# Kernel optimization log

Hardware: AMD Instinct MI355X
Metric: run time of the kernel (lower is better)

The kernel has to match this reference:

```python
import jax, jax.numpy as jnp
import numpy as np

LATENT = 128
K = 1024          # num_embeddings
LENGTH = 128
HID = 200         # LSTM hidden
IN = 768
COND = 1536


def setup_inputs() -> dict:
    key = jax.random.key(0)
    ks = jax.random.split(key, 16)
    B = 256
    x = jax.random.normal(ks[0], (B, 1, LENGTH, IN), dtype=jnp.float32)
    condition = jax.random.normal(ks[1], (B, 1, LENGTH, COND), dtype=jnp.float32)
    noise = jax.random.normal(ks[2], (B, IN), dtype=jnp.float32)
    s = 0.05
    # LSTM params (PyTorch gate order: i, f, g, o)
    W_ih = jax.random.normal(ks[3], (4 * HID, IN), dtype=jnp.float32) * s
    W_hh = jax.random.normal(ks[4], (4 * HID, HID), dtype=jnp.float32) * s
    b_ih = jax.random.normal(ks[5], (4 * HID,), dtype=jnp.float32) * s
    b_hh = jax.random.normal(ks[6], (4 * HID,), dtype=jnp.float32) * s
    # encoder fc: HID -> LATENT
    W_enc = jax.random.normal(ks[7], (LATENT, HID), dtype=jnp.float32) * s
    b_enc = jnp.zeros((LATENT,), dtype=jnp.float32)
    # codebook, uniform(-1/K, 1/K) as in the module
    emb = jax.random.uniform(ks[8], (K, LATENT), minval=-1.0 / K, maxval=1.0 / K, dtype=jnp.float32)
    # decoder MLP
    D1_IN = LATENT + COND + IN  # 2432
    W1 = jax.random.normal(ks[9], (200, D1_IN), dtype=jnp.float32) * s
    b1 = jnp.zeros((200,), dtype=jnp.float32)
    W2 = jax.random.normal(ks[10], (400, 200), dtype=jnp.float32) * s
    b2 = jnp.zeros((400,), dtype=jnp.float32)
    W3 = jax.random.normal(ks[11], (IN, 400), dtype=jnp.float32) * s
    b3 = jnp.zeros((IN,), dtype=jnp.float32)
    return {"x": x, "condition": condition, "noise": noise,
            "W_ih": W_ih, "W_hh": W_hh, "b_ih": b_ih, "b_hh": b_hh,
            "W_enc": W_enc, "b_enc": b_enc, "emb": emb,
            "W1": W1, "b1": b1, "W2": W2, "b2": b2, "W3": W3, "b3": b3}


def _lstm_last_h(xs, W_ih, W_hh, b_ih, b_hh):
    # xs: [B, T, IN] -> final hidden state [B, HID]
    B = xs.shape[0]
    h0 = jnp.zeros((B, HID), dtype=xs.dtype)
    c0 = jnp.zeros((B, HID), dtype=xs.dtype)
    # precompute input projections for all timesteps: [T, B, 4H]
    gates_x = jnp.einsum('bti,gi->tbg', xs, W_ih) + b_ih + b_hh

    def step(carry, gx):
        h, c = carry
        g = gx + h @ W_hh.T  # [B, 4H]
        i, f, gg, o = jnp.split(g, 4, axis=-1)
        c = jax.nn.sigmoid(f) * c + jax.nn.sigmoid(i) * jnp.tanh(gg)
        h = jax.nn.sigmoid(o) * jnp.tanh(c)
        return (h, c), None

    (h, _), _ = jax.lax.scan(step, (h0, c0), gates_x)
    return h


def reference(x, condition, noise, W_ih, W_hh, b_ih, b_hh, W_enc, b_enc, emb,
              W1, b1, W2, b2, W3, b3):
    B = x.shape[0]
    # Encoder
    xs = x.reshape(B, -1, IN)                      # [B, T, 768]
    h = _lstm_last_h(xs, W_ih, W_hh, b_ih, b_hh)   # [B, 200]
    z_e = h @ W_enc.T + b_enc                      # [B, latent]
    # VectorQuantizer: squared-distance argmin + gather
    d = (jnp.sum(z_e * z_e, axis=-1, keepdims=True)
         + jnp.sum(emb * emb, axis=1)
         - 2.0 * z_e @ emb.T)                      # [B, K]
    indices = jnp.argmin(d, axis=-1)               # [B]
    z_q = emb[indices]                             # [B, latent]
    # Decoder (forward uses z_q directly)
    L = LENGTH
    z = jnp.broadcast_to(z_q[:, None, None, :], (B, 1, L, LATENT))
    n = jnp.broadcast_to(noise[:, None, None, :], (B, 1, L, IN))
    zc = jnp.concatenate([z, condition, n], axis=-1)  # [B,1,L,2432]
    h1 = jax.nn.relu(zc @ W1.T + b1)
    h2 = jax.nn.relu(h1 @ W2.T + b2)
    out = jax.nn.sigmoid(h2 @ W3.T + b3)
    return out.reshape(-1, 1, L, IN)
```

## Files before the change

### kernel.cpp

```cpp
#include <hip/hip_runtime.h>
#include <hip/hip_fp16.h>
#include <math.h>

typedef unsigned short u16;
typedef u16 u16x8 __attribute__((ext_vector_type(8)));
typedef __bf16 bf16x8 __attribute__((ext_vector_type(8)));
typedef float f32x4 __attribute__((ext_vector_type(4)));

#define HID 200
#define G4H 800
#define TLEN 128
#define LATENT 128
#define NCODES 1024
#define DIN 768
#define DCOND 1536
#define NB 256
#define MROWS (NB * TLEN)
#define LDG 896
#define LDH1 256
#define LDH2 512
#define NOUT 768

__device__ __forceinline__ u16 f2b(float f) {
  union { float f; unsigned u; } v; v.f = f;
  unsigned r = v.u + 0x7fffu + ((v.u >> 16) & 1u);
  return (u16)(r >> 16);
}
__device__ __forceinline__ float b2f(u16 h) {
  union { unsigned u; float f; } v; v.u = ((unsigned)h) << 16;
  return v.f;
}
__device__ __forceinline__ float sigf(float x) { return 1.f / (1.f + __expf(-x)); }
__device__ __forceinline__ float tanh_fast(float x) {
  return 1.f - 2.f / (__expf(2.f * x) + 1.f);
}

__device__ __forceinline__ void gl16(const void* g, void* l) {
  __builtin_amdgcn_global_load_lds(
      (const __attribute__((address_space(1))) void*)g,
      (__attribute__((address_space(3))) void*)l, 16, 0, 0);
}

__device__ __forceinline__ unsigned cvtpk(float a, float b) {
  unsigned r;
  asm("v_cvt_pk_bf16_f32 %0, %1, %2" : "=v"(r) : "v"(a), "v"(b));
  return r;
}

__global__ void cvt_pad(const float* __restrict__ src, u16* __restrict__ dst,
                        int nr, int nc, int lds, int col0, int NRp, int KP) {
  int i = blockIdx.x * blockDim.x + threadIdx.x;
  if (i >= NRp * KP) return;
  int r = i / KP, c = i - r * KP;
  float v = (r < nr && c < nc) ? src[(size_t)r * lds + col0 + c] : 0.f;
  dst[i] = f2b(v);
}

__global__ void pad_f32(const float* __restrict__ src, float* __restrict__ dst,
                        int n, int npad) {
  int i = blockIdx.x * blockDim.x + threadIdx.x;
  if (i < npad) dst[i] = (i < n) ? src[i] : 0.f;
}

__global__ void pack_whh(const float* __restrict__ Whh, __half2* __restrict__ Wt2,
                         const float* __restrict__ b_ih, const float* __restrict__ b_hh,
                         float* __restrict__ biasc) {
  int i = blockIdx.x * blockDim.x + threadIdx.x;
  if (i < 200 * 400) {
    int k = i / 400, r = i - k * 400;
    Wt2[i] = __floats2half2_rn(Whh[(size_t)r * HID + k], Whh[(size_t)(r + 400) * HID + k]);
  }
  if (i < G4H) biasc[i] = b_ih[i] + b_hh[i];
}

enum { EPI_GATES = 0, EPI_H1 = 1, EPI_H2 = 2, EPI_OUT = 3 };

__device__ __forceinline__ f32x4 mfma16(bf16x8 a, bf16x8 b, f32x4 c) {
  return __builtin_amdgcn_mfma_f32_16x16x32_bf16(a, b, c, 0, 0, 0);
}

template<bool AF32, int EPI>
__global__ __launch_bounds__(256) void gemm_bf16(
    const void* __restrict__ Ap, const u16* __restrict__ Bp,
    void* __restrict__ Cp, int K, int ldc, const float* __restrict__ bias) {
  __shared__ __attribute__((aligned(16))) char AsRaw[AF32 ? 128 * 32 * 4 : 128 * 32 * 2];
  __shared__ __attribute__((aligned(16))) u16 Bs[128 * 32];
  float* Asf = (float*)AsRaw;
  u16* As16 = (u16*)AsRaw;

  const int t = threadIdx.x;
  const int tileN = blockIdx.x * 128;
  const int tileM = blockIdx.y * 128;
  const int l = t & 63;
  const int w = t >> 6;
  const int wr = (w >> 1) * 64;
  const int wc = (w & 1) * 64;
  const int fr = l & 15;
  const int fg = l >> 4;

  const u16* bsrc[2];
  u16* bdst[2];
#pragma unroll
  for (int j = 0; j < 2; ++j) {
    int tb = w * 1024 + j * 4096 + (t & 63) * 16;
    int row = tb >> 6, gd = (tb >> 4) & 3;
    bsrc[j] = Bp + (size_t)(tileN + row) * K + ((gd ^ ((row >> 1) & 3)) << 3);
    bdst[j] = Bs + w * 512 + j * 2048;
  }
  const float* asrcF[4];
  float* adstF[4];
  const u16* asrcH[2];
  u16* adstH[2];
  if constexpr (AF32) {
#pragma unroll
    for (int j = 0; j < 4; ++j) {
      int tb = w * 1024 + j * 4096 + (t & 63) * 16;
      int row = tb >> 7, gd = (tb >> 4) & 7;
      asrcF[j] = (const float*)Ap + (size_t)(tileM + row) * K + ((gd ^ (row & 7)) << 2);
      adstF[j] = Asf + w * 256 + j * 1024;
    }
  } else {
#pragma unroll
    for (int j = 0; j < 2; ++j) {
      int tb = w * 1024 + j * 4096 + (t & 63) * 16;
      int row = tb >> 6, gd = (tb >> 4) & 3;
      asrcH[j] = (const u16*)Ap + (size_t)(tileM + row) * K + ((gd ^ ((row >> 1) & 3)) << 3);
      adstH[j] = As16 + w * 512 + j * 2048;
    }
  }

  f32x4 acc[4][4];
#pragma unroll
  for (int m = 0; m < 4; ++m)
#pragma unroll
    for (int n = 0; n < 4; ++n) {
      f32x4 z = {0.f, 0.f, 0.f, 0.f};
      acc[m][n] = z;
    }

  for (int k0 = 0; k0 < K; k0 += 32) {
#pragma unroll
    for (int j = 0; j < 2; ++j) { gl16(bsrc[j], bdst[j]); bsrc[j] += 32; }
    if constexpr (AF32) {
#pragma unroll
      for (int j = 0; j < 4; ++j) { gl16(asrcF[j], adstF[j]); asrcF[j] += 32; }
    } else {
#pragma unroll
      for (int j = 0; j < 2; ++j) { gl16(asrcH[j], adstH[j]); asrcH[j] += 32; }
    }
    __syncthreads();

    bf16x8 av[4], bv[4];
#pragma unroll
    for (int m = 0; m < 4; ++m) {
      const int row = wr + m * 16 + fr;
      if constexpr (AF32) {
        const int g0 = (2 * fg) ^ (row & 7);
        const int g1 = (2 * fg + 1) ^ (row & 7);
        float4 p0 = *(const float4*)(Asf + row * 32 + g0 * 4);
        float4 p1 = *(const float4*)(Asf + row * 32 + g1 * 4);
        uint4 u;
        u.x = cvtpk(p0.x, p0.y); u.y = cvtpk(p0.z, p0.w);
        u.z = cvtpk(p1.x, p1.y); u.w = cvtpk(p1.z, p1.w);
        av[m] = __builtin_bit_cast(bf16x8, u);
      } else {
        const int g = fg ^ ((row >> 1) & 3);
        av[m] = __builtin_bit_cast(bf16x8, *(const u16x8*)(As16 + row * 32 + g * 8));
      }
    }
#pragma unroll
    for (int n = 0; n < 4; ++n) {
      const int row = wc + n * 16 + fr;
      const int g = fg ^ ((row >> 1) & 3);
      bv[n] = __builtin_bit_cast(bf16x8, *(const u16x8*)(Bs + row * 32 + g * 8));
    }
#pragma unroll
    for (int m = 0; m < 4; ++m)
#pragma unroll
      for (int n = 0; n < 4; ++n)
        acc[m][n] = mfma16(av[m], bv[n], acc[m][n]);
    __syncthreads();
  }

#pragma unroll
  for (int m = 0; m < 4; ++m) {
#pragma unroll
    for (int n = 0; n < 4; ++n) {
      const int gcol = tileN + wc + n * 16 + fr;
      const int growb = tileM + wr + m * 16 + fg * 4;
#pragma unroll
      for (int r = 0; r < 4; ++r) {
        const int grow = growb + r;
        float v = acc[m][n][r];
        if constexpr (EPI == EPI_GATES) {
          ((u16*)Cp)[(size_t)grow * ldc + gcol] = f2b(v);
        } else if constexpr (EPI == EPI_H1) {
          v += bias[(grow >> 7) * 256 + gcol];
          v = fmaxf(v, 0.f);
          ((u16*)Cp)[(size_t)grow * ldc + gcol] = f2b(v);
        } else if constexpr (EPI == EPI_H2) {
          v += bias[gcol];
          v = fmaxf(v, 0.f);
          ((u16*)Cp)[(size_t)grow * ldc + gcol] = f2b(v);
        } else {
          v += bias[gcol];
          ((float*)Cp)[(size_t)grow * ldc + gcol] = sigf(v);
        }
      }
    }
  }
}

__global__ __launch_bounds__(448, 1) void lstm_enc(
    const u16* __restrict__ gates, const unsigned* __restrict__ Wt2,
    const float* __restrict__ biasc,
    const float* __restrict__ Wenc, const float* __restrict__ b_enc,
    const float* __restrict__ emb, const float* __restrict__ W1,
    const float* __restrict__ b1, const float* __restrict__ noise,
    float* __restrict__ p1) {
  __shared__ __attribute__((aligned(16))) __half sh_h[208];
  __shared__ __attribute__((aligned(16))) float sh_hf[HID];
  __shared__ float sh_g[G4H];
  __shared__ __attribute__((aligned(16))) float sh_ze[LATENT];
  __shared__ float sh_zq[LATENT];
  __shared__ float sh_rd[448];
  __shared__ int sh_ri[448];
  const int r = threadIdx.x;
  const int b = blockIdx.x;
  const bool active = (r < 400);

  unsigned wv[200];
  float biasA = 0.f, biasB = 0.f;
  if (active) {
#pragma unroll
    for (int k = 0; k < 200; ++k) wv[k] = Wt2[(size_t)k * 400 + r];
    biasA = biasc[r];
    biasB = biasc[r + 400];
  }
  if (r < HID) sh_h[r] = __float2half(0.f);
  float c = 0.f;
  float gvA = 0.f, gvB = 0.f;
  if (active) {
    gvA = b2f(gates[(size_t)(b * TLEN) * LDG + r]);
    gvB = b2f(gates[(size_t)(b * TLEN) * LDG + r + 400]);
  }
  __syncthreads();

  for (int t = 0; t < TLEN; ++t) {
    float gvA_n = 0.f, gvB_n = 0.f;
    if (active && t + 1 < TLEN) {
      gvA_n = b2f(gates[(size_t)(b * TLEN + t + 1) * LDG + r]);
      gvB_n = b2f(gates[(size_t)(b * TLEN + t + 1) * LDG + r + 400]);
    }

    if (active) {
      unsigned a0 = 0, a1 = 0, a2 = 0, a3 = 0;
      const uint4* H = (const uint4*)sh_h;
#pragma unroll
      for (int q4 = 0; q4 < 25; ++q4) {
        uint4 hv = H[q4];
        asm("v_pk_fma_f16 %0, %1, %2, %0 op_sel:[0,0,0] op_sel_hi:[1,0,1]"
            : "+v"(a0) : "v"(wv[8 * q4 + 0]), "v"(hv.x));
        asm("v_pk_fma_f16 %0, %1, %2, %0 op_sel:[0,1,0] op_sel_hi:[1,1,1]"
            : "+v"(a1) : "v"(wv[8 * q4 + 1]), "v"(hv.x));
        asm("v_pk_fma_f16 %0, %1, %2, %0 op_sel:[0,0,0] op_sel_hi:[1,0,1]"
            : "+v"(a2) : "v"(wv[8 * q4 + 2]), "v"(hv.y));
        asm("v_pk_fma_f16 %0, %1, %2, %0 op_sel:[0,1,0] op_sel_hi:[1,1,1]"
            : "+v"(a3) : "v"(wv[8 * q4 + 3]), "v"(hv.y));
        asm("v_pk_fma_f16 %0, %1, %2, %0 op_sel:[0,0,0] op_sel_hi:[1,0,1]"
            : "+v"(a0) : "v"(wv[8 * q4 + 4]), "v"(hv.z));
        asm("v_pk_fma_f16 %0, %1, %2, %0 op_sel:[0,1,0] op_sel_hi:[1,1,1]"
            : "+v"(a1) : "v"(wv[8 * q4 + 5]), "v"(hv.z));
        asm("v_pk_fma_f16 %0, %1, %2, %0 op_sel:[0,0,0] op_sel_hi:[1,0,1]"
            : "+v"(a2) : "v"(wv[8 * q4 + 6]), "v"(hv.w));
        asm("v_pk_fma_f16 %0, %1, %2, %0 op_sel:[0,1,0] op_sel_hi:[1,1,1]"
            : "+v"(a3) : "v"(wv[8 * q4 + 7]), "v"(hv.w));
      }
      __half2 s = __hadd2(__hadd2(__builtin_bit_cast(__half2, a0), __builtin_bit_cast(__half2, a1)),
                          __hadd2(__builtin_bit_cast(__half2, a2), __builtin_bit_cast(__half2, a3)));
      sh_g[r] = biasA + gvA + __low2float(s);
      sh_g[r + 400] = biasB + gvB + __high2float(s);
    }
    __syncthreads();
    if (r < HID) {
      float gi = sh_g[r], gf = sh_g[HID + r], gg = sh_g[2 * HID + r], go = sh_g[3 * HID + r];
      c = sigf(gf) * c + sigf(gi) * tanh_fast(gg);
      float h = sigf(go) * tanh_fast(c);
      sh_h[r] = __float2half(h);
      sh_hf[r] = h;
    }
    __syncthreads();
    gvA = gvA_n; gvB = gvB_n;
  }

  if (r < LATENT) {
    float z = b_enc[r];
#pragma unroll 4
    for (int k = 0; k < HID; ++k) z = fmaf(Wenc[(size_t)r * HID + k], sh_hf[k], z);
    sh_ze[r] = z;
  }
  __syncthreads();

  float best = INFINITY; int bi = 0;
  for (int k = r; k < NCODES; k += 448) {
    float d = 0.f;
#pragma unroll
    for (int q = 0; q < LATENT / 4; ++q) {
      float4 e = *(const float4*)&emb[(size_t)k * LATENT + q * 4];
      float4 z = *(const float4*)&sh_ze[q * 4];
      d += e.x * (e.x - 2.f * z.x) + e.y * (e.y - 2.f * z.y)
         + e.z * (e.z - 2.f * z.z) + e.w * (e.w - 2.f * z.w);
    }
    if (d < best) { best = d; bi = k; }
  }
  sh_rd[r] = best; sh_ri[r] = bi;
  __syncthreads();
  for (int s = 256; s > 0; s >>= 1) {
    if (r < s && r + s < 448) {
      float od = sh_rd[r + s]; int oi = sh_ri[r + s];
      if (od < sh_rd[r] || (od == sh_rd[r] && oi < sh_ri[r])) { sh_rd[r] = od; sh_ri[r] = oi; }
    }
    __syncthreads();
  }
  const int kmin = sh_ri[0];
  if (r < LATENT) sh_zq[r] = emb[(size_t)kmin * LATENT + r];
  __syncthreads();

  if (r < 256) {
    float v = 0.f;
    if (r < HID) {
      v = b1[r];
      const float* wrow = W1 + (size_t)r * 2432;
#pragma unroll 4
      for (int d = 0; d < LATENT; ++d) v = fmaf(wrow[d], sh_zq[d], v);
      const float* nz = noise + (size_t)b * DIN;
#pragma unroll 4
      for (int d = 0; d < DIN; ++d) v = fmaf(wrow[1664 + d], nz[d], v);
    }
    p1[b * 256 + r] = v;
  }
}

extern "C" void kernel_launch(void* const* d_in, const int* in_sizes, int n_in,
                              void* d_out, int out_size, void* d_ws, size_t ws_size,
                              hipStream_t stream) {
  const float* x     = (const float*)d_in[0];
  const float* cond  = (const float*)d_in[1];
  const float* noise = (const float*)d_in[2];
  const float* W_ih  = (const float*)d_in[3];
  const float* W_hh  = (const float*)d_in[4];
  const float* b_ih  = (const float*)d_in[5];
  const float* b_hh  = (const float*)d_in[6];
  const float* W_enc = (const float*)d_in[7];
  const float* b_enc = (const float*)d_in[8];
  const float* emb   = (const float*)d_in[9];
  const float* W1    = (const float*)d_in[10];
  const float* b1    = (const float*)d_in[11];
  const float* W2    = (const float*)d_in[12];
  const float* b2    = (const float*)d_in[13];
  const float* W3    = (const float*)d_in[14];
  const float* b3    = (const float*)d_in[15];

  char* ws = (char*)d_ws;
  size_t off = 0;
  auto alloc = [&](size_t bytes) -> void* {
    void* p = ws + off; off += (bytes + 255) & ~(size_t)255; return p;
  };
  u16*      W_ihb = (u16*)alloc((size_t)896 * 768 * 2);
  u16*      W1cb  = (u16*)alloc((size_t)256 * 1536 * 2);
  u16*      W2b   = (u16*)alloc((size_t)512 * 256 * 2);
  u16*      W3b   = (u16*)alloc((size_t)768 * 512 * 2);
  float*    b2p   = (float*)alloc(512 * 4);
  unsigned* Wt2   = (unsigned*)alloc((size_t)200 * 400 * 4);
  float*    biasc = (float*)alloc(G4H * 4);
  u16*      gates = (u16*)alloc((size_t)MROWS * LDG * 2);
  float*    p1    = (float*)alloc(256 * 256 * 4);
  u16*      h1    = (u16*)alloc((size_t)MROWS * LDH1 * 2);
  u16*      h2    = (u16*)alloc((size_t)MROWS * LDH2 * 2);

  cvt_pad<<<dim3((896 * 768 + 255) / 256), 256, 0, stream>>>(W_ih, W_ihb, 800, 768, 768, 0, 896, 768);
  cvt_pad<<<dim3((256 * 1536 + 255) / 256), 256, 0, stream>>>(W1, W1cb, 200, 1536, 2432, 128, 256, 1536);
  cvt_pad<<<dim3((512 * 256 + 255) / 256), 256, 0, stream>>>(W2, W2b, 400, 200, 200, 0, 512, 256);
  cvt_pad<<<dim3((768 * 512 + 255) / 256), 256, 0, stream>>>(W3, W3b, 768, 400, 400, 0, 768, 512);
  pad_f32<<<dim3(2), 256, 0, stream>>>(b2, b2p, 400, 512);
  pack_whh<<<dim3((200 * 400 + 255) / 256), 256, 0, stream>>>(W_hh, (__half2*)Wt2, b_ih, b_hh, biasc);

  gemm_bf16<true, EPI_GATES><<<dim3(LDG / 128, MROWS / 128), 256, 0, stream>>>(
      x, W_ihb, gates, 768, LDG, nullptr);

  lstm_enc<<<dim3(NB), 448, 0, stream>>>(gates, Wt2, biasc, W_enc, b_enc,
                                         emb, W1, b1, noise, p1);

  gemm_bf16<true, EPI_H1><<<dim3(LDH1 / 128, MROWS / 128), 256, 0, stream>>>(
      cond, W1cb, h1, DCOND, LDH1, p1);
  gemm_bf16<false, EPI_H2><<<dim3(LDH2 / 128, MROWS / 128), 256, 0, stream>>>(
      h1, W2b, h2, LDH1, LDH2, b2p);
  gemm_bf16<false, EPI_OUT><<<dim3(NOUT / 128, MROWS / 128), 256, 0, stream>>>(
      h2, W3b, (float*)d_out, LDH2, NOUT, b3);
}
```

Baseline: 577.4 us.

## Batch LSTM recurrence across 16 sequences per block using bf16 MFMA

Replaces the per-sequence LSTM kernel, which ran 256 blocks doing fp16 packed FMAs against register-resident weights, with a scan kernel in which each block handles 16 batch rows. The recurrent matmul runs as 16x16x32 bf16 MFMAs with W_hh prepacked into fragment layout and held in registers, and h is double-buffered in LDS. The gates GEMM epilogue now folds in the bias and writes a time-major, gate-padded layout so each step reads coalesced rows. The VQ and decoder projection move to a separate kernel. The scan now uses only 16 blocks, so most of the GPU sits idle during the serial recurrence, and the hidden state is rounded to bf16 each step, which costs precision.

```diff
diff --git a/kernel.cpp b/kernel.cpp
--- a/kernel.cpp
+++ b/kernel.cpp
@@ -1,5 +1,4 @@
 #include <hip/hip_runtime.h>
-#include <hip/hip_fp16.h>
 #include <math.h>
 
 typedef unsigned short u16;
@@ -47,6 +46,16 @@
   return r;
 }
 
+__device__ __forceinline__ f32x4 gx4(uint2 u) {
+  union { unsigned q; float f; } a;
+  f32x4 r;
+  a.q = u.x << 16;          r.x = a.f;
+  a.q = u.x & 0xFFFF0000u;  r.y = a.f;
+  a.q = u.y << 16;          r.z = a.f;
+  a.q = u.y & 0xFFFF0000u;  r.w = a.f;
+  return r;
+}
+
 __global__ void cvt_pad(const float* __restrict__ src, u16* __restrict__ dst,
                         int nr, int nc, int lds, int col0, int NRp, int KP) {
   int i = blockIdx.x * blockDim.x + threadIdx.x;
@@ -62,15 +71,34 @@
   if (i < npad) dst[i] = (i < n) ? src[i] : 0.f;
 }
 
-__global__ void pack_whh(const float* __restrict__ Whh, __half2* __restrict__ Wt2,
-                         const float* __restrict__ b_ih, const float* __restrict__ b_hh,
-                         float* __restrict__ biasc) {
+__global__ void bias_pack(const float* __restrict__ b_ih, const float* __restrict__ b_hh,
+                          float* __restrict__ biasc) {
   int i = blockIdx.x * blockDim.x + threadIdx.x;
-  if (i < 200 * 400) {
-    int k = i / 400, r = i - k * 400;
-    Wt2[i] = __floats2half2_rn(Whh[(size_t)r * HID + k], Whh[(size_t)(r + 400) * HID + k]);
-  }
-  if (i < G4H) biasc[i] = b_ih[i] + b_hh[i];
+  if (i < LDG) biasc[i] = (i < G4H) ? (b_ih[i] + b_hh[i]) : 0.f;
+}
+
+__global__ void pack_wf(const float* __restrict__ Whh, uint4* __restrict__ Wf) {
+  int i = blockIdx.x * blockDim.x + threadIdx.x;
+  if (i >= 56 * 64) return;
+  int l = i & 63, rest = i >> 6;
+  int f = rest % 7, tt = (rest / 7) & 7, w = rest / 56;
+  int gate = tt >> 1, s = tt & 1;
+  int u = w * 32 + s * 16 + (l & 15);
+  int kbase = f * 32 + (l >> 4) * 8;
+  unsigned out[4];
+#pragma unroll
+  for (int d = 0; d < 4; ++d) {
+    unsigned lo = 0, hi = 0;
+    int k0 = kbase + 2 * d, k1 = k0 + 1;
+    if (u < HID) {
+      const float* row = Whh + (size_t)(gate * HID + u) * HID;
+      if (k0 < HID) lo = f2b(row[k0]);
+      if (k1 < HID) hi = f2b(row[k1]);
+    }
+    out[d] = lo | (hi << 16);
+  }
+  uint4 o; o.x = out[0]; o.y = out[1]; o.z = out[2]; o.w = out[3];
+  Wf[i] = o;
 }
 
 enum { EPI_GATES = 0, EPI_H1 = 1, EPI_H2 = 2, EPI_OUT = 3 };
@@ -193,7 +221,12 @@
         const int grow = growb + r;
         float v = acc[m][n][r];
         if constexpr (EPI == EPI_GATES) {
-          ((u16*)Cp)[(size_t)grow * ldc + gcol] = f2b(v);
+          v += bias[gcol];
+          int tt = grow & 127, bb = grow >> 7;
+          int rp;
+          if (gcol < G4H) rp = (gcol / HID) * 224 + gcol % HID;
+          else { int j = gcol - G4H; rp = (j / 24) * 224 + 200 + j % 24; }
+          ((u16*)Cp)[((size_t)tt * 256 + bb) * LDG + rp] = f2b(v);
         } else if constexpr (EPI == EPI_H1) {
           v += bias[(grow >> 7) * 256 + gcol];
           v = fmaxf(v, 0.f);
@@ -211,87 +244,114 @@
   }
 }
 
-__global__ __launch_bounds__(448, 1) void lstm_enc(
-    const u16* __restrict__ gates, const unsigned* __restrict__ Wt2,
-    const float* __restrict__ biasc,
+__global__ __launch_bounds__(448) void lstm_scan(
+    const u16* __restrict__ gatesT,
+    const uint4* __restrict__ Wf,
+    float* __restrict__ h_final) {
+  __shared__ __attribute__((aligned(16))) uint4 hbuf[2][7][64];
+  const int tid = threadIdx.x;
+  const int l = tid & 63;
+  const int w = tid >> 6;
+  const int fg = l >> 4;
+  const int fr = l & 15;
+  const int bglob = blockIdx.x * 16 + fr;
+
+  bf16x8 wf[8][7];
+  {
+    const uint4* wp = Wf + (size_t)w * 56 * 64 + l;
+#pragma unroll
+    for (int tt = 0; tt < 8; ++tt)
+#pragma unroll
+      for (int f = 0; f < 7; ++f)
+        wf[tt][f] = __builtin_bit_cast(bf16x8, wp[(tt * 7 + f) * 64]);
+  }
+  for (int i = tid; i < 7 * 64; i += 448) {
+    uint4 z = {0, 0, 0, 0};
+    hbuf[0][i >> 6][i & 63] = z;
+  }
+  float c[8];
+#pragma unroll
+  for (int i = 0; i < 8; ++i) c[i] = 0.f;
+  float hfin[8];
+
+  const u16* gp = gatesT + ((size_t)0 * 256 + bglob) * LDG + w * 32 + fg * 4;
+  uint2 gx[8];
+#pragma unroll
+  for (int tt = 0; tt < 8; ++tt)
+    gx[tt] = *(const uint2*)(gp + (tt >> 1) * 224 + (tt & 1) * 16);
+  __syncthreads();
+
+  for (int t = 0; t < TLEN; ++t) {
+    const int cur = t & 1, nxt = cur ^ 1;
+    uint2 gxn[8];
+    gp += 256 * LDG;
+    if (t + 1 < TLEN) {
+#pragma unroll
+      for (int tt = 0; tt < 8; ++tt)
+        gxn[tt] = *(const uint2*)(gp + (tt >> 1) * 224 + (tt & 1) * 16);
+    }
+    bf16x8 hf[7];
+#pragma unroll
+    for (int f = 0; f < 7; ++f)
+      hf[f] = __builtin_bit_cast(bf16x8, hbuf[cur][f][l]);
+    f32x4 acc[8];
+#pragma unroll
+    for (int tt = 0; tt < 8; ++tt) acc[tt] = gx4(gx[tt]);
+#pragma unroll
+    for (int f = 0; f < 7; ++f)
+#pragma unroll
+      for (int tt = 0; tt < 8; ++tt)
+        acc[tt] = mfma16(wf[tt][f], hf[f], acc[tt]);
+#pragma unroll
+    for (int s = 0; s < 2; ++s) {
+      float hh[4];
+#pragma unroll
+      for (int reg = 0; reg < 4; ++reg) {
+        float gi = acc[0 + s][reg], gf = acc[2 + s][reg];
+        float gg = acc[4 + s][reg], go = acc[6 + s][reg];
+        int ci = s * 4 + reg;
+        c[ci] = sigf(gf) * c[ci] + sigf(gi) * tanh_fast(gg);
+        float h = sigf(go) * tanh_fast(c[ci]);
+        int u = w * 32 + s * 16 + fg * 4 + reg;
+        hh[reg] = (u < HID) ? h : 0.f;
+        hfin[ci] = hh[reg];
+      }
+      uint2 pk;
+      pk.x = cvtpk(hh[0], hh[1]);
+      pk.y = cvtpk(hh[2], hh[3]);
+      const int g = s * 2 + (fg >> 1);
+      *(uint2*)((char*)&hbuf[nxt][w][0] + (g * 16 + fr) * 16 + (fg & 1) * 8) = pk;
+    }
+#pragma unroll
+    for (int tt = 0; tt < 8; ++tt) gx[tt] = gxn[tt];
+    __syncthreads();
+  }
+
+#pragma unroll
+  for (int s = 0; s < 2; ++s)
+#pragma unroll
+    for (int reg = 0; reg < 4; ++reg) {
+      int u = w * 32 + s * 16 + fg * 4 + reg;
+      if (u < HID) h_final[(size_t)bglob * HID + u] = hfin[s * 4 + reg];
+    }
+}
+
+__global__ __launch_bounds__(256) void enc_vq(
+    const float* __restrict__ h_final,
     const float* __restrict__ Wenc, const float* __restrict__ b_enc,
     const float* __restrict__ emb, const float* __restrict__ W1,
     const float* __restrict__ b1, const float* __restrict__ noise,
     float* __restrict__ p1) {
-  __shared__ __attribute__((aligned(16))) __half sh_h[208];
   __shared__ __attribute__((aligned(16))) float sh_hf[HID];
-  __shared__ float sh_g[G4H];
   __shared__ __attribute__((aligned(16))) float sh_ze[LATENT];
   __shared__ float sh_zq[LATENT];
-  __shared__ float sh_rd[448];
-  __shared__ int sh_ri[448];
+  __shared__ float sh_rd[256];
+  __shared__ int sh_ri[256];
   const int r = threadIdx.x;
   const int b = blockIdx.x;
-  const bool active = (r < 400);
-
-  unsigned wv[200];
-  float biasA = 0.f, biasB = 0.f;
-  if (active) {
-#pragma unroll
-    for (int k = 0; k < 200; ++k) wv[k] = Wt2[(size_t)k * 400 + r];
-    biasA = biasc[r];
-    biasB = biasc[r + 400];
-  }
-  if (r < HID) sh_h[r] = __float2half(0.f);
-  float c = 0.f;
-  float gvA = 0.f, gvB = 0.f;
-  if (active) {
-    gvA = b2f(gates[(size_t)(b * TLEN) * LDG + r]);
-    gvB = b2f(gates[(size_t)(b * TLEN) * LDG + r + 400]);
-  }
+
+  if (r < HID) sh_hf[r] = h_final[(size_t)b * HID + r];
   __syncthreads();
-
-  for (int t = 0; t < TLEN; ++t) {
-    float gvA_n = 0.f, gvB_n = 0.f;
-    if (active && t + 1 < TLEN) {
-      gvA_n = b2f(gates[(size_t)(b * TLEN + t + 1) * LDG + r]);
-      gvB_n = b2f(gates[(size_t)(b * TLEN + t + 1) * LDG + r + 400]);
-    }
-
-    if (active) {
-      unsigned a0 = 0, a1 = 0, a2 = 0, a3 = 0;
-      const uint4* H = (const uint4*)sh_h;
-#pragma unroll
-      for (int q4 = 0; q4 < 25; ++q4) {
-        uint4 hv = H[q4];
-        asm("v_pk_fma_f16 %0, %1, %2, %0 op_sel:[0,0,0] op_sel_hi:[1,0,1]"
-            : "+v"(a0) : "v"(wv[8 * q4 + 0]), "v"(hv.x));
-        asm("v_pk_fma_f16 %0, %1, %2, %0 op_sel:[0,1,0] op_sel_hi:[1,1,1]"
-            : "+v"(a1) : "v"(wv[8 * q4 + 1]), "v"(hv.x));
-        asm("v_pk_fma_f16 %0, %1, %2, %0 op_sel:[0,0,0] op_sel_hi:[1,0,1]"
-            : "+v"(a2) : "v"(wv[8 * q4 + 2]), "v"(hv.y));
-        asm("v_pk_fma_f16 %0, %1, %2, %0 op_sel:[0,1,0] op_sel_hi:[1,1,1]"
-            : "+v"(a3) : "v"(wv[8 * q4 + 3]), "v"(hv.y));
-        asm("v_pk_fma_f16 %0, %1, %2, %0 op_sel:[0,0,0] op_sel_hi:[1,0,1]"
-            : "+v"(a0) : "v"(wv[8 * q4 + 4]), "v"(hv.z));
-        asm("v_pk_fma_f16 %0, %1, %2, %0 op_sel:[0,1,0] op_sel_hi:[1,1,1]"
-            : "+v"(a1) : "v"(wv[8 * q4 + 5]), "v"(hv.z));
-        asm("v_pk_fma_f16 %0, %1, %2, %0 op_sel:[0,0,0] op_sel_hi:[1,0,1]"
-            : "+v"(a2) : "v"(wv[8 * q4 + 6]), "v"(hv.w));
-        asm("v_pk_fma_f16 %0, %1, %2, %0 op_sel:[0,1,0] op_sel_hi:[1,1,1]"
-            : "+v"(a3) : "v"(wv[8 * q4 + 7]), "v"(hv.w));
-      }
-      __half2 s = __hadd2(__hadd2(__builtin_bit_cast(__half2, a0), __builtin_bit_cast(__half2, a1)),
-                          __hadd2(__builtin_bit_cast(__half2, a2), __builtin_bit_cast(__half2, a3)));
-      sh_g[r] = biasA + gvA + __low2float(s);
-      sh_g[r + 400] = biasB + gvB + __high2float(s);
-    }
-    __syncthreads();
-    if (r < HID) {
-      float gi = sh_g[r], gf = sh_g[HID + r], gg = sh_g[2 * HID + r], go = sh_g[3 * HID + r];
-      c = sigf(gf) * c + sigf(gi) * tanh_fast(gg);
-      float h = sigf(go) * tanh_fast(c);
-      sh_h[r] = __float2half(h);
-      sh_hf[r] = h;
-    }
-    __syncthreads();
-    gvA = gvA_n; gvB = gvB_n;
-  }
 
   if (r < LATENT) {
     float z = b_enc[r];
@@ -302,7 +362,7 @@
   __syncthreads();
 
   float best = INFINITY; int bi = 0;
-  for (int k = r; k < NCODES; k += 448) {
+  for (int k = r; k < NCODES; k += 256) {
     float d = 0.f;
 #pragma unroll
     for (int q = 0; q < LATENT / 4; ++q) {
@@ -315,8 +375,8 @@
   }
   sh_rd[r] = best; sh_ri[r] = bi;
   __syncthreads();
-  for (int s = 256; s > 0; s >>= 1) {
-    if (r < s && r + s < 448) {
+  for (int s = 128; s > 0; s >>= 1) {
+    if (r < s) {
       float od = sh_rd[r + s]; int oi = sh_ri[r + s];
       if (od < sh_rd[r] || (od == sh_rd[r] && oi < sh_ri[r])) { sh_rd[r] = od; sh_ri[r] = oi; }
     }
@@ -326,19 +386,17 @@
   if (r < LATENT) sh_zq[r] = emb[(size_t)kmin * LATENT + r];
   __syncthreads();
 
-  if (r < 256) {
-    float v = 0.f;
-    if (r < HID) {
-      v = b1[r];
-      const float* wrow = W1 + (size_t)r * 2432;
+  float v = 0.f;
+  if (r < HID) {
+    v = b1[r];
+    const float* wrow = W1 + (size_t)r * 2432;
 #pragma unroll 4
-      for (int d = 0; d < LATENT; ++d) v = fmaf(wrow[d], sh_zq[d], v);
-      const float* nz = noise + (size_t)b * DIN;
+    for (int d = 0; d < LATENT; ++d) v = fmaf(wrow[d], sh_zq[d], v);
+    const float* nz = noise + (size_t)b * DIN;
 #pragma unroll 4
-      for (int d = 0; d < DIN; ++d) v = fmaf(wrow[1664 + d], nz[d], v);
-    }
-    p1[b * 256 + r] = v;
-  }
+    for (int d = 0; d < DIN; ++d) v = fmaf(wrow[1664 + d], nz[d], v);
+  }
+  p1[b * 256 + r] = v;
 }
 
 extern "C" void kernel_launch(void* const* d_in, const int* in_sizes, int n_in,
@@ -366,30 +424,33 @@
   auto alloc = [&](size_t bytes) -> void* {
     void* p = ws + off; off += (bytes + 255) & ~(size_t)255; return p;
   };
-  u16*      W_ihb = (u16*)alloc((size_t)896 * 768 * 2);
-  u16*      W1cb  = (u16*)alloc((size_t)256 * 1536 * 2);
-  u16*      W2b   = (u16*)alloc((size_t)512 * 256 * 2);
-  u16*      W3b   = (u16*)alloc((size_t)768 * 512 * 2);
-  float*    b2p   = (float*)alloc(512 * 4);
-  unsigned* Wt2   = (unsigned*)alloc((size_t)200 * 400 * 4);
-  float*    biasc = (float*)alloc(G4H * 4);
-  u16*      gates = (u16*)alloc((size_t)MROWS * LDG * 2);
-  float*    p1    = (float*)alloc(256 * 256 * 4);
-  u16*      h1    = (u16*)alloc((size_t)MROWS * LDH1 * 2);
-  u16*      h2    = (u16*)alloc((size_t)MROWS * LDH2 * 2);
+  u16*   W_ihb = (u16*)alloc((size_t)896 * 768 * 2);
+  u16*   W1cb  = (u16*)alloc((size_t)256 * 1536 * 2);
+  u16*   W2b   = (u16*)alloc((size_t)512 * 256 * 2);
+  u16*   W3b   = (u16*)alloc((size_t)768 * 512 * 2);
+  float* b2p   = (float*)alloc(512 * 4);
+  uint4* Wf    = (uint4*)alloc((size_t)56 * 64 * 16);
+  float* biasc = (float*)alloc(LDG * 4);
+  u16*   gatesT = (u16*)alloc((size_t)MROWS * LDG * 2);
+  float* h_fin = (float*)alloc((size_t)NB * HID * 4);
+  float* p1    = (float*)alloc(256 * 256 * 4);
+  u16*   h1    = (u16*)alloc((size_t)MROWS * LDH1 * 2);
+  u16*   h2    = (u16*)alloc((size_t)MROWS * LDH2 * 2);
 
   cvt_pad<<<dim3((896 * 768 + 255) / 256), 256, 0, stream>>>(W_ih, W_ihb, 800, 768, 768, 0, 896, 768);
   cvt_pad<<<dim3((256 * 1536 + 255) / 256), 256, 0, stream>>>(W1, W1cb, 200, 1536, 2432, 128, 256, 1536);
   cvt_pad<<<dim3((512 * 256 + 255) / 256), 256, 0, stream>>>(W2, W2b, 400, 200, 200, 0, 512, 256);
   cvt_pad<<<dim3((768 * 512 + 255) / 256), 256, 0, stream>>>(W3, W3b, 768, 400, 400, 0, 768, 512);
   pad_f32<<<dim3(2), 256, 0, stream>>>(b2, b2p, 400, 512);
-  pack_whh<<<dim3((200 * 400 + 255) / 256), 256, 0, stream>>>(W_hh, (__half2*)Wt2, b_ih, b_hh, biasc);
+  bias_pack<<<dim3(4), 256, 0, stream>>>(b_ih, b_hh, biasc);
+  pack_wf<<<dim3(14), 256, 0, stream>>>(W_hh, Wf);
 
   gemm_bf16<true, EPI_GATES><<<dim3(LDG / 128, MROWS / 128), 256, 0, stream>>>(
-      x, W_ihb, gates, 768, LDG, nullptr);
-
-  lstm_enc<<<dim3(NB), 448, 0, stream>>>(gates, Wt2, biasc, W_enc, b_enc,
-                                         emb, W1, b1, noise, p1);
+      x, W_ihb, gatesT, 768, LDG, biasc);
+
+  lstm_scan<<<dim3(16), 448, 0, stream>>>(gatesT, Wf, h_fin);
+
+  enc_vq<<<dim3(NB), 256, 0, stream>>>(h_fin, W_enc, b_enc, emb, W1, b1, noise, p1);
 
   gemm_bf16<true, EPI_H1><<<dim3(LDH1 / 128, MROWS / 128), 256, 0, stream>>>(
       cond, W1cb, h1, DCOND, LDH1, p1);
```

New measurement: 1.006 ms. 74.2% more time.
